# Optimization experiments

Measured on AMD Instinct MI355X. Metric: run time of the kernel, lower is better.

The kernel has to match this reference:

```python
import jax, jax.numpy as jnp
import numpy as np

NUM_BITS = 8
VMIN, VMAX = 0.0, 1.0
THRESH = 4.0
K_SYN = 32


def gray_code_encode(x):
    # (batch, features) -> (batch, features*NUM_BITS) binary float bits
    norm = (jnp.clip(x, VMIN, VMAX) - VMIN) / (VMAX - VMIN)
    levels = jnp.round(norm * (2 ** NUM_BITS - 1)).astype(jnp.int32)
    gray = levels ^ (levels >> 1)
    bit_pos = jnp.arange(NUM_BITS, dtype=jnp.int32)
    bits = ((gray[..., None] >> bit_pos) & 1).astype(jnp.float32)
    return bits.reshape(x.shape[0], -1)


def _make_sparse_weight(key, n_neurons, prev_size):
    # k random synapses per neuron with +/-1 weights (rest zero), as in
    # _initialise_layer_weights (standard, non-dynamic path)
    kc, ks = jax.random.split(key)
    cols = jax.random.randint(kc, (n_neurons, K_SYN), 0, prev_size)
    signs = jax.random.randint(ks, (n_neurons, K_SYN), 0, 2).astype(jnp.float32) * 2 - 1
    rows = jnp.broadcast_to(jnp.arange(n_neurons)[:, None], (n_neurons, K_SYN))
    return jnp.zeros((n_neurons, prev_size), jnp.float32).at[rows, cols].set(signs)


def setup_inputs() -> dict:
    key = jax.random.key(0)
    kx, k0, k1, k2, ko = jax.random.split(key, 5)
    batch, feat = 512, 256
    hidden, classes, n_hidden_layers = 4096, 1000, 3
    enc = feat * NUM_BITS  # 2048
    x = jax.random.uniform(kx, (batch, feat), dtype=jnp.float32)
    W0 = _make_sparse_weight(k0, hidden, enc)
    W1 = _make_sparse_weight(k1, hidden, hidden)
    W2 = _make_sparse_weight(k2, hidden, hidden)
    out_w = jax.random.normal(ko, (n_hidden_layers, hidden, classes), dtype=jnp.float32) * 0.01
    return {"x": x, "W0": W0, "W1": W1, "W2": W2, "out_w": out_w}


def reference(x, W0, W1, W2, out_w):
    prev = gray_code_encode(x)  # (b, enc)
    out = jnp.zeros((x.shape[0], out_w.shape[-1]), jnp.float32)
    for i, W in enumerate((W0, W1, W2)):
        z = prev @ W.T                                  # (b, hidden)
        prev = (z >= THRESH).astype(jnp.float32)        # binary activation
        out = out + prev @ out_w[i]                     # accumulate per-layer
    return out
```

## Files before the change

kernel.cpp:

```cpp
#include <hip/hip_runtime.h>
#include <stdint.h>

typedef unsigned long long u64;
typedef __attribute__((ext_vector_type(8))) short bf16x8;
typedef __attribute__((ext_vector_type(4))) float f32x4;
typedef __attribute__((ext_vector_type(4))) unsigned u32x4;

#define BATCH 512
#define FEAT 256
#define ENC 2048
#define HID 4096
#define CLS 1000
#define KTOT 12288
#define KSPLIT 768

#define OFF_ENC2   0
#define OFF_ACT2   131072
#define OFF_TABLE  917504
#define OFF_SGN    1703936
#define OFF_WT     2097152

static __device__ inline unsigned short f2bf(float f) {
    unsigned u = __float_as_uint(f);
    return (unsigned short)((u + 0x7FFFu + ((u >> 16) & 1u)) >> 16);
}

static __device__ inline void gld16(const void* g, void* s) {
    __builtin_amdgcn_global_load_lds((const __attribute__((address_space(1))) void*)g,
                                     (__attribute__((address_space(3))) void*)s, 16, 0, 0);
}

__global__ void __launch_bounds__(256)
k_prep(const float* __restrict__ x, u64* __restrict__ enc2,
       const float* __restrict__ W0, const float* __restrict__ W1,
       const float* __restrict__ W2,
       uint16_t* __restrict__ table, unsigned* __restrict__ bits,
       const float* __restrict__ out_w, short* __restrict__ wt,
       float* __restrict__ out) {
    __shared__ short tile[64 * 68];
    __shared__ int cnt4[4];
    __shared__ int lneg[4];
    int bid = blockIdx.x;
    int t = threadIdx.x;
    int lane = t & 63;
    int wv = t >> 6;

    if (bid < 512) {
        int oidx = bid * 256 + t;
        if (oidx < (BATCH * CLS) / 4) {
            f32x4 z = {0.f, 0.f, 0.f, 0.f};
            *(f32x4*)&out[(size_t)oidx * 4] = z;
        }
        int wid = bid * 4 + wv;
        int f = wid >> 3, bg = wid & 7;
        float v = x[(size_t)(bg * 64 + lane) * FEAT + f];
        v = fminf(fmaxf(v, 0.0f), 1.0f);
        int lev = (int)rintf(v * 255.0f);
        unsigned gray = (unsigned)(lev ^ (lev >> 1));
        u64 w = 0;
        #pragma unroll
        for (int bit = 0; bit < 8; ++bit) {
            u64 m = __ballot((gray >> bit) & 1u);
            if (lane == bit) w = m;
        }
        if (lane < 8) enc2[(size_t)bg * ENC + f * 8 + lane] = w;
        return;
    }
    if (bid < 5632) {
        int wsid = (bid - 512) * 4 + wv;
        int row, base, cidx;
        if (wsid < HID) { row = wsid; base = 0; cidx = wv; }
        else {
            int w2 = wsid - HID;
            row = HID + (w2 >> 1);
            base = (w2 & 1) * 2048;
            cidx = wv >> 1;
        }
        uint16_t* te = table + (size_t)row * 32;
        if (lane < 8) ((u64*)te)[lane] = 0;
        if (t < 4) { cnt4[t] = 0; lneg[t] = 0; }
        __syncthreads();
        const float* Wr;
        if (row < HID)          Wr = W0 + (size_t)row * ENC;
        else if (row < 2 * HID) Wr = W1 + (size_t)(row - HID) * HID + base;
        else                    Wr = W2 + (size_t)(row - 2 * HID) * HID + base;
        const u32x4* p4 = (const u32x4*)Wr;
        u32x4 v[8];
        #pragma unroll
        for (int j = 0; j < 8; ++j) v[j] = __builtin_nontemporal_load(p4 + j * 64 + lane);
        #pragma unroll
        for (int j = 0; j < 8; ++j) {
            unsigned a0 = v[j].x, a1 = v[j].y, a2 = v[j].z, a3 = v[j].w;
            if (a0 | a1 | a2 | a3) {
                int col0 = base + j * 256 + lane * 4;
                if (a0) { int s = atomicAdd(&cnt4[cidx], 1); te[s] = (uint16_t)col0;
                          if (a0 >> 31) atomicOr(&lneg[cidx], (int)(1u << s)); }
                if (a1) { int s = atomicAdd(&cnt4[cidx], 1); te[s] = (uint16_t)(col0 + 1);
                          if (a1 >> 31) atomicOr(&lneg[cidx], (int)(1u << s)); }
                if (a2) { int s = atomicAdd(&cnt4[cidx], 1); te[s] = (uint16_t)(col0 + 2);
                          if (a2 >> 31) atomicOr(&lneg[cidx], (int)(1u << s)); }
                if (a3) { int s = atomicAdd(&cnt4[cidx], 1); te[s] = (uint16_t)(col0 + 3);
                          if (a3 >> 31) atomicOr(&lneg[cidx], (int)(1u << s)); }
            }
        }
        __syncthreads();
        if (lane == 0) {
            int cnt = cnt4[cidx];
            unsigned nb = (unsigned)lneg[cidx];
            unsigned vb = (cnt >= 32) ? 0xFFFFFFFFu : ((1u << cnt) - 1u);
            uint2 pr; pr.x = nb; pr.y = vb;
            *(uint2*)(bits + (size_t)row * 2) = pr;
        }
        return;
    }
    {
        int b2 = bid - 5632;
        int kt = b2 % 192, ct = b2 / 192;
        int k0 = kt * 64, c0 = ct * 64;
        {
            int rrow = t >> 4, c4 = t & 15;
            int c = c0 + c4 * 4;
            #pragma unroll
            for (int rd = 0; rd < 4; ++rd) {
                int kl = rd * 16 + rrow;
                f32x4 vv;
                if (c < CLS)
                    vv = __builtin_nontemporal_load(
                        (const f32x4*)&out_w[(size_t)(k0 + kl) * CLS + c]);
                else { vv.x = 0.0f; vv.y = 0.0f; vv.z = 0.0f; vv.w = 0.0f; }
                short* d = &tile[kl * 68 + c4 * 4];
                d[0] = (short)f2bf(vv.x); d[1] = (short)f2bf(vv.y);
                d[2] = (short)f2bf(vv.z); d[3] = (short)f2bf(vv.w);
            }
        }
        __syncthreads();
        {
            int chunk = t & 7, cl2 = t >> 3;
            #pragma unroll
            for (int rd = 0; rd < 2; ++rd) {
                int c_local = rd * 32 + cl2;
                int c = c0 + c_local;
                unsigned s8[8];
                #pragma unroll
                for (int j = 0; j < 8; ++j)
                    s8[j] = (unsigned)(unsigned short)tile[(chunk * 8 + j) * 68 + c_local];
                uint4 pk;
                pk.x = s8[0] | (s8[1] << 16);
                pk.y = s8[2] | (s8[3] << 16);
                pk.z = s8[4] | (s8[5] << 16);
                pk.w = s8[6] | (s8[7] << 16);
                *(uint4*)&wt[(size_t)c * KTOT + k0 + ((chunk ^ (c & 7)) * 8)] = pk;
            }
        }
    }
}

static __device__ __forceinline__ u64 unit_csa(
    const u64* __restrict__ prow,
    const uint16_t* __restrict__ table_l, const unsigned* __restrict__ bits_l, int n) {
    const uint4* tq = (const uint4*)(table_l + (size_t)n * 32);
    uint4 cwa[4] = {tq[0], tq[1], tq[2], tq[3]};
    uint2 bv = *(const uint2*)(bits_l + (size_t)n * 2);
    unsigned negb = bv.x, valb = bv.y;

    u64 P[4][4];
    #pragma unroll
    for (int k = 0; k < 4; ++k) {
        unsigned w0 = cwa[k].x, w1 = cwa[k].y, w2 = cwa[k].z, w3 = cwa[k].w;
        unsigned cc[8] = { w0 & 0xFFFFu, w0 >> 16, w1 & 0xFFFFu, w1 >> 16,
                           w2 & 0xFFFFu, w2 >> 16, w3 & 0xFFFFu, w3 >> 16 };
        u64 u[8];
        #pragma unroll
        for (int e = 0; e < 8; ++e) {
            int j = (k << 3) + e;
            u64 w = prow[cc[e]];
            u64 negm = 0ull - (u64)((negb >> j) & 1u);
            u64 vm   = 0ull - (u64)((valb >> j) & 1u);
            u[e] = (w ^ negm) & vm;
        }
        u64 s0, c0, s1, c1, s2, c2, b0, c3, t2, d0, b1, d1;
        { u64 t = u[0] ^ u[1]; s0 = t ^ u[2]; c0 = (u[0] & u[1]) | (u[2] & t); }
        { u64 t = u[3] ^ u[4]; s1 = t ^ u[5]; c1 = (u[3] & u[4]) | (u[5] & t); }
        s2 = u[6] ^ u[7]; c2 = u[6] & u[7];
        { u64 t = s0 ^ s1; b0 = t ^ s2; c3 = (s0 & s1) | (s2 & t); }
        { u64 t = c0 ^ c1; t2 = t ^ c2; d0 = (c0 & c1) | (c2 & t); }
        b1 = t2 ^ c3; d1 = t2 & c3;
        P[k][0] = b0; P[k][1] = b1; P[k][2] = d0 ^ d1; P[k][3] = d0 & d1;
    }
    u64 A[5], B[5], U[6];
    { u64 c;
      { u64 t = P[0][0] ^ P[1][0]; A[0] = t; c = P[0][0] & P[1][0]; }
      #pragma unroll
      for (int i = 1; i < 4; ++i) {
          u64 t = P[0][i] ^ P[1][i]; A[i] = t ^ c; c = (P[0][i] & P[1][i]) | (c & t); }
      A[4] = c; }
    { u64 c;
      { u64 t = P[2][0] ^ P[3][0]; B[0] = t; c = P[2][0] & P[3][0]; }
      #pragma unroll
      for (int i = 1; i < 4; ++i) {
          u64 t = P[2][i] ^ P[3][i]; B[i] = t ^ c; c = (P[2][i] & P[3][i]) | (c & t); }
      B[4] = c; }
    { u64 c;
      { u64 t = A[0] ^ B[0]; U[0] = t; c = A[0] & B[0]; }
      #pragma unroll
      for (int i = 1; i < 5; ++i) {
          u64 t = A[i] ^ B[i]; U[i] = t ^ c; c = (A[i] & B[i]) | (c & t); }
      U[5] = c; }
    int K = 60 - __popc(negb & valb);
    u64 c = 0;
    #pragma unroll
    for (int i = 0; i < 6; ++i) {
        u64 ki = 0ull - (u64)((K >> i) & 1);
        u64 t = U[i] ^ ki;
        c = (U[i] & ki) | (c & t);
    }
    return c;
}

__global__ void __launch_bounds__(64)
k_layer(const u64* __restrict__ prev2, int Kwords,
        const uint16_t* __restrict__ table_l, const unsigned* __restrict__ bits_l,
        u64* __restrict__ actout) {
    int unit = blockIdx.x;
    int lane = threadIdx.x;
    int g = unit >> 3, bg = unit & 7;
    int n = (g << 6) + lane;
    u64 c = unit_csa(prev2 + (size_t)bg * Kwords, table_l, bits_l, n);
    actout[(size_t)bg * HID + n] = c;
}

__global__ void __launch_bounds__(256)
k_gemm_atomic(const u64* __restrict__ act2, const short* __restrict__ wt,
              float* __restrict__ out) {
    __shared__ __attribute__((aligned(16))) short As[128 * 64];
    __shared__ __attribute__((aligned(16))) short Bs[128 * 64];
    int bid = blockIdx.x;
    int mt = bid & 3, nt = (bid >> 2) & 7, ks = bid >> 5;
    int tid = threadIdx.x, lane = tid & 63;
    int wv = tid >> 6, waveM = wv & 1, waveN = wv >> 1;
    int quad = lane >> 4, cl = lane & 15;
    f32x4 acc[4][4] = {};
    const char* Bb = (const char*)(wt + (size_t)nt * 128 * KTOT + ks * KSPLIT);
    int r = tid >> 3, sub = tid & 7;
    for (int kk = 0; kk < KSPLIT; kk += 64) {
        #pragma unroll
        for (int rd = 0; rd < 4; ++rd) {
            size_t go = (size_t)(r + rd * 32) * (KTOT * 2) + kk * 2 + sub * 16;
            gld16(Bb + go, &Bs[(tid + rd * 256) * 8]);
        }
        {
            int kabs = ks * KSPLIT + kk;
            int l = kabs >> 12, nk = kabs & 4095;
            #pragma unroll
            for (int i = 0; i < 4; ++i) {
                int item = i * 256 + tid;
                int rr = item >> 3, gg = item & 7;
                const u64* w8 = act2 + ((size_t)(l * 8 + mt * 2 + (rr >> 6))) * HID + nk + gg * 8;
                int bl = rr & 63;
                unsigned sh[8];
                #pragma unroll
                for (int j = 0; j < 8; ++j)
                    sh[j] = (unsigned)((w8[j] >> bl) & 1ull) * 0x3F80u;
                uint4 pk;
                pk.x = sh[0] | (sh[1] << 16);
                pk.y = sh[2] | (sh[3] << 16);
                pk.z = sh[4] | (sh[5] << 16);
                pk.w = sh[6] | (sh[7] << 16);
                *(uint4*)&As[rr * 64 + ((gg ^ (rr & 7)) * 8)] = pk;
            }
        }
        __syncthreads();
        #pragma unroll
        for (int s = 0; s < 2; ++s) {
            int xr = ((s * 4 + quad) ^ (cl & 7)) * 8;
            bf16x8 af[4], bfr[4];
            #pragma unroll
            for (int mf = 0; mf < 4; ++mf)
                af[mf] = *(const bf16x8*)&As[(waveM * 64 + mf * 16 + cl) * 64 + xr];
            #pragma unroll
            for (int nf = 0; nf < 4; ++nf)
                bfr[nf] = *(const bf16x8*)&Bs[(waveN * 64 + nf * 16 + cl) * 64 + xr];
            #pragma unroll
            for (int mf = 0; mf < 4; ++mf)
                #pragma unroll
                for (int nf = 0; nf < 4; ++nf)
                    acc[mf][nf] = __builtin_amdgcn_mfma_f32_16x16x32_bf16(
                        af[mf], bfr[nf], acc[mf][nf], 0, 0, 0);
        }
        __syncthreads();
    }
    #pragma unroll
    for (int mf = 0; mf < 4; ++mf)
        #pragma unroll
        for (int nf = 0; nf < 4; ++nf) {
            int cp = nt * 128 + waveN * 64 + nf * 16 + cl;
            if (cp < CLS) {
                #pragma unroll
                for (int rr = 0; rr < 4; ++rr) {
                    int mg = mt * 128 + waveM * 64 + mf * 16 + quad * 4 + rr;
                    atomicAdd(&out[(size_t)mg * CLS + cp], acc[mf][nf][rr]);
                }
            }
        }
}

extern "C" void kernel_launch(void* const* d_in, const int* in_sizes, int n_in,
                              void* d_out, int out_size, void* d_ws, size_t ws_size,
                              hipStream_t stream) {
    const float* x     = (const float*)d_in[0];
    const float* W0    = (const float*)d_in[1];
    const float* W1    = (const float*)d_in[2];
    const float* W2    = (const float*)d_in[3];
    const float* out_w = (const float*)d_in[4];
    float* out = (float*)d_out;
    char* ws = (char*)d_ws;

    u64*       enc2   = (u64*)(ws + OFF_ENC2);
    u64*       act2   = (u64*)(ws + OFF_ACT2);
    uint16_t*  table  = (uint16_t*)(ws + OFF_TABLE);
    unsigned*  bits   = (unsigned*)(ws + OFF_SGN);
    short*     wt     = (short*)(ws + OFF_WT);

    hipLaunchKernelGGL(k_prep, dim3(8704), dim3(256), 0, stream,
                       x, enc2, W0, W1, W2, table, bits, out_w, wt, out);
    hipLaunchKernelGGL(k_layer, dim3(512), dim3(64), 0, stream,
                       enc2, ENC, table, bits, act2);
    hipLaunchKernelGGL(k_layer, dim3(512), dim3(64), 0, stream,
                       act2, HID, table + (size_t)HID * 32, bits + (size_t)HID * 2,
                       act2 + 8 * HID);
    hipLaunchKernelGGL(k_layer, dim3(512), dim3(64), 0, stream,
                       act2 + 8 * HID, HID, table + (size_t)2 * HID * 32,
                       bits + (size_t)2 * HID * 2, act2 + 16 * HID);
    hipLaunchKernelGGL(k_gemm_atomic, dim3(512), dim3(256), 0, stream,
                       act2, wt, out);
}
```

Before: 271.2 us.

## Build sparse tables with ballot compaction and shrink final GEMM M tile

The weight-table build now uses one wavefront per row and wave-wide ballot/popcount prefix sums in place of LDS atomics and block barriers, with W1/W2 rows handled in two passes by the same wave. Negative-sign bits are merged with shuffle-xor. The prep grid shrinks accordingly. The final atomic GEMM switches from 128x128 tiles to 64x128 tiles (one batch group per block), doubling the block count to 1024 for more parallelism, at the cost of rereading the B operand twice as often.

```diff
diff --git a/kernel.cpp b/kernel.cpp
--- a/kernel.cpp
+++ b/kernel.cpp
@@ -38,8 +38,6 @@
        const float* __restrict__ out_w, short* __restrict__ wt,
        float* __restrict__ out) {
     __shared__ short tile[64 * 68];
-    __shared__ int cnt4[4];
-    __shared__ int lneg[4];
     int bid = blockIdx.x;
     int t = threadIdx.x;
     int lane = t & 63;
@@ -66,55 +64,50 @@
         if (lane < 8) enc2[(size_t)bg * ENC + f * 8 + lane] = w;
         return;
     }
-    if (bid < 5632) {
-        int wsid = (bid - 512) * 4 + wv;
-        int row, base, cidx;
-        if (wsid < HID) { row = wsid; base = 0; cidx = wv; }
-        else {
-            int w2 = wsid - HID;
-            row = HID + (w2 >> 1);
-            base = (w2 & 1) * 2048;
-            cidx = wv >> 1;
-        }
+    if (bid < 3584) {
+        int row = (bid - 512) * 4 + wv;
+        const float* Wr; int npass;
+        if (row < HID)          { Wr = W0 + (size_t)row * ENC;             npass = 1; }
+        else if (row < 2 * HID) { Wr = W1 + (size_t)(row - HID) * HID;     npass = 2; }
+        else                    { Wr = W2 + (size_t)(row - 2 * HID) * HID; npass = 2; }
         uint16_t* te = table + (size_t)row * 32;
-        if (lane < 8) ((u64*)te)[lane] = 0;
-        if (t < 4) { cnt4[t] = 0; lneg[t] = 0; }
-        __syncthreads();
-        const float* Wr;
-        if (row < HID)          Wr = W0 + (size_t)row * ENC;
-        else if (row < 2 * HID) Wr = W1 + (size_t)(row - HID) * HID + base;
-        else                    Wr = W2 + (size_t)(row - 2 * HID) * HID + base;
-        const u32x4* p4 = (const u32x4*)Wr;
-        u32x4 v[8];
-        #pragma unroll
-        for (int j = 0; j < 8; ++j) v[j] = __builtin_nontemporal_load(p4 + j * 64 + lane);
-        #pragma unroll
-        for (int j = 0; j < 8; ++j) {
-            unsigned a0 = v[j].x, a1 = v[j].y, a2 = v[j].z, a3 = v[j].w;
-            if (a0 | a1 | a2 | a3) {
-                int col0 = base + j * 256 + lane * 4;
-                if (a0) { int s = atomicAdd(&cnt4[cidx], 1); te[s] = (uint16_t)col0;
-                          if (a0 >> 31) atomicOr(&lneg[cidx], (int)(1u << s)); }
-                if (a1) { int s = atomicAdd(&cnt4[cidx], 1); te[s] = (uint16_t)(col0 + 1);
-                          if (a1 >> 31) atomicOr(&lneg[cidx], (int)(1u << s)); }
-                if (a2) { int s = atomicAdd(&cnt4[cidx], 1); te[s] = (uint16_t)(col0 + 2);
-                          if (a2 >> 31) atomicOr(&lneg[cidx], (int)(1u << s)); }
-                if (a3) { int s = atomicAdd(&cnt4[cidx], 1); te[s] = (uint16_t)(col0 + 3);
-                          if (a3 >> 31) atomicOr(&lneg[cidx], (int)(1u << s)); }
-            }
-        }
-        __syncthreads();
+        unsigned cnt = 0, mynegs = 0;
+        u64 ltmask = (1ull << lane) - 1ull;
+        for (int p = 0; p < npass; ++p) {
+            const u32x4* p4 = (const u32x4*)Wr + p * 512 + lane;
+            u32x4 v[8];
+            #pragma unroll
+            for (int j = 0; j < 8; ++j) v[j] = __builtin_nontemporal_load(p4 + j * 64);
+            #pragma unroll
+            for (int j = 0; j < 8; ++j) {
+                int col0 = (p * 8 + j) * 256 + lane * 4;
+                unsigned aa[4] = {v[j].x, v[j].y, v[j].z, v[j].w};
+                #pragma unroll
+                for (int c = 0; c < 4; ++c) {
+                    unsigned a = aa[c];
+                    u64 m = __ballot(a != 0u);
+                    if (a) {
+                        int slot = (int)cnt + (int)__popcll(m & ltmask);
+                        te[slot] = (uint16_t)(col0 + c);
+                        if (a >> 31) mynegs |= 1u << slot;
+                    }
+                    cnt += (unsigned)__popcll(m);
+                }
+            }
+        }
+        #pragma unroll
+        for (int off = 32; off; off >>= 1) mynegs |= __shfl_xor(mynegs, off);
+        if (lane >= (int)cnt && lane < 32) te[lane] = 0;
         if (lane == 0) {
-            int cnt = cnt4[cidx];
-            unsigned nb = (unsigned)lneg[cidx];
-            unsigned vb = (cnt >= 32) ? 0xFFFFFFFFu : ((1u << cnt) - 1u);
-            uint2 pr; pr.x = nb; pr.y = vb;
+            uint2 pr;
+            pr.x = mynegs;
+            pr.y = (cnt >= 32) ? 0xFFFFFFFFu : ((1u << cnt) - 1u);
             *(uint2*)(bits + (size_t)row * 2) = pr;
         }
         return;
     }
     {
-        int b2 = bid - 5632;
+        int b2 = bid - 3584;
         int kt = b2 % 192, ct = b2 / 192;
         int k0 = kt * 64, c0 = ct * 64;
         {
@@ -232,14 +225,14 @@
 __global__ void __launch_bounds__(256)
 k_gemm_atomic(const u64* __restrict__ act2, const short* __restrict__ wt,
               float* __restrict__ out) {
-    __shared__ __attribute__((aligned(16))) short As[128 * 64];
+    __shared__ __attribute__((aligned(16))) short As[64 * 64];
     __shared__ __attribute__((aligned(16))) short Bs[128 * 64];
     int bid = blockIdx.x;
-    int mt = bid & 3, nt = (bid >> 2) & 7, ks = bid >> 5;
+    int nt = bid & 7, ks = (bid >> 3) & 15, mt = bid >> 7;
     int tid = threadIdx.x, lane = tid & 63;
-    int wv = tid >> 6, waveM = wv & 1, waveN = wv >> 1;
+    int wv = tid >> 6;
     int quad = lane >> 4, cl = lane & 15;
-    f32x4 acc[4][4] = {};
+    f32x4 acc[4][2] = {};
     const char* Bb = (const char*)(wt + (size_t)nt * 128 * KTOT + ks * KSPLIT);
     int r = tid >> 3, sub = tid & 7;
     for (int kk = 0; kk < KSPLIT; kk += 64) {
@@ -252,15 +245,14 @@
             int kabs = ks * KSPLIT + kk;
             int l = kabs >> 12, nk = kabs & 4095;
             #pragma unroll
-            for (int i = 0; i < 4; ++i) {
+            for (int i = 0; i < 2; ++i) {
                 int item = i * 256 + tid;
                 int rr = item >> 3, gg = item & 7;
-                const u64* w8 = act2 + ((size_t)(l * 8 + mt * 2 + (rr >> 6))) * HID + nk + gg * 8;
-                int bl = rr & 63;
+                const u64* w8 = act2 + ((size_t)(l * 8 + mt)) * HID + nk + gg * 8;
                 unsigned sh[8];
                 #pragma unroll
                 for (int j = 0; j < 8; ++j)
-                    sh[j] = (unsigned)((w8[j] >> bl) & 1ull) * 0x3F80u;
+                    sh[j] = (unsigned)((w8[j] >> rr) & 1ull) * 0x3F80u;
                 uint4 pk;
                 pk.x = sh[0] | (sh[1] << 16);
                 pk.y = sh[2] | (sh[3] << 16);
@@ -273,17 +265,17 @@
         #pragma unroll
         for (int s = 0; s < 2; ++s) {
             int xr = ((s * 4 + quad) ^ (cl & 7)) * 8;
-            bf16x8 af[4], bfr[4];
+            bf16x8 af[4], bfr[2];
             #pragma unroll
             for (int mf = 0; mf < 4; ++mf)
-                af[mf] = *(const bf16x8*)&As[(waveM * 64 + mf * 16 + cl) * 64 + xr];
-            #pragma unroll
-            for (int nf = 0; nf < 4; ++nf)
-                bfr[nf] = *(const bf16x8*)&Bs[(waveN * 64 + nf * 16 + cl) * 64 + xr];
+                af[mf] = *(const bf16x8*)&As[(mf * 16 + cl) * 64 + xr];
+            #pragma unroll
+            for (int nf = 0; nf < 2; ++nf)
+                bfr[nf] = *(const bf16x8*)&Bs[(wv * 32 + nf * 16 + cl) * 64 + xr];
             #pragma unroll
             for (int mf = 0; mf < 4; ++mf)
                 #pragma unroll
-                for (int nf = 0; nf < 4; ++nf)
+                for (int nf = 0; nf < 2; ++nf)
                     acc[mf][nf] = __builtin_amdgcn_mfma_f32_16x16x32_bf16(
                         af[mf], bfr[nf], acc[mf][nf], 0, 0, 0);
         }
@@ -292,12 +284,12 @@
     #pragma unroll
     for (int mf = 0; mf < 4; ++mf)
         #pragma unroll
-        for (int nf = 0; nf < 4; ++nf) {
-            int cp = nt * 128 + waveN * 64 + nf * 16 + cl;
+        for (int nf = 0; nf < 2; ++nf) {
+            int cp = nt * 128 + wv * 32 + nf * 16 + cl;
             if (cp < CLS) {
                 #pragma unroll
                 for (int rr = 0; rr < 4; ++rr) {
-                    int mg = mt * 128 + waveM * 64 + mf * 16 + quad * 4 + rr;
+                    int mg = mt * 64 + mf * 16 + quad * 4 + rr;
                     atomicAdd(&out[(size_t)mg * CLS + cp], acc[mf][nf][rr]);
                 }
             }
@@ -321,7 +313,7 @@
     unsigned*  bits   = (unsigned*)(ws + OFF_SGN);
     short*     wt     = (short*)(ws + OFF_WT);
 
-    hipLaunchKernelGGL(k_prep, dim3(8704), dim3(256), 0, stream,
+    hipLaunchKernelGGL(k_prep, dim3(6656), dim3(256), 0, stream,
                        x, enc2, W0, W1, W2, table, bits, out_w, wt, out);
     hipLaunchKernelGGL(k_layer, dim3(512), dim3(64), 0, stream,
                        enc2, ENC, table, bits, act2);
@@ -331,6 +323,6 @@
     hipLaunchKernelGGL(k_layer, dim3(512), dim3(64), 0, stream,
                        act2 + 8 * HID, HID, table + (size_t)2 * HID * 32,
                        bits + (size_t)2 * HID * 2, act2 + 16 * HID);
-    hipLaunchKernelGGL(k_gemm_atomic, dim3(512), dim3(256), 0, stream,
+    hipLaunchKernelGGL(k_gemm_atomic, dim3(1024), dim3(256), 0, stream,
                        act2, wt, out);
 }
```

After: 270.4 us. About the same (-0.3%).
